# Optimization experiments

Hardware: AMD Instinct MI355X
Metric: run time of the kernel (lower is better)

## Reference

```python
import jax, jax.numpy as jnp
import numpy as np
from jax import lax

D_MODEL = 512
D_STATE = 16
D_CONV = 4
EXPAND = 2
D_INNER = EXPAND * D_MODEL          # 1024
DT_RANK = (D_MODEL + 15) // 16      # 32 (ceil(d_model/16))
BATCH = 8
SEQLEN = 2048


def _mamba_params(key):
    ks = jax.random.split(key, 6)
    s = 0.02
    return {
        'in_w':   jax.random.normal(ks[0], (2 * D_INNER, D_MODEL)) * s,
        'conv_w': jax.random.normal(ks[1], (D_INNER, D_CONV)) * s,
        'conv_b': jnp.zeros((D_INNER,)),
        'xp_w':   jax.random.normal(ks[2], (DT_RANK + 2 * D_STATE, D_INNER)) * s,
        'dt_w':   jax.random.normal(ks[3], (D_INNER, DT_RANK)) * s,
        'dt_b':   jax.random.uniform(ks[4], (D_INNER,), minval=-4.0, maxval=-2.0),
        'A_log':  jnp.log(jnp.tile(jnp.arange(1, D_STATE + 1, dtype=jnp.float32), (D_INNER, 1))),
        'Dp':     jnp.ones((D_INNER,)),
        'out_w':  jax.random.normal(ks[5], (D_MODEL, D_INNER)) * s,
    }


def setup_inputs() -> dict:
    key = jax.random.key(0)
    kx, kf, kb, kl1, kl2 = jax.random.split(key, 5)
    pf = _mamba_params(kf)
    pb = _mamba_params(kb)
    inp = {'x': jax.random.normal(kx, (BATCH, SEQLEN, D_MODEL), dtype=jnp.float32)}
    for name, v in pf.items():
        inp['f_' + name] = v
    for name, v in pb.items():
        inp['b_' + name] = v
    inp['lin_w'] = jax.random.normal(kl1, (D_MODEL, 2 * D_MODEL)) * 0.02
    inp['lin_b'] = jnp.zeros((D_MODEL,))
    return inp


def _mamba(x, in_w, conv_w, conv_b, xp_w, dt_w, dt_b, A_log, Dp, out_w):
    # x: (B, L, D_MODEL)
    Bsz = x.shape[0]
    xz = x @ in_w.T                                  # (B, L, 2*D_INNER)
    xi, z = jnp.split(xz, 2, axis=-1)
    # causal depthwise conv over time
    xc = jnp.transpose(xi, (0, 2, 1))                # (B, D_INNER, L)
    xc = lax.conv_general_dilated(
        xc, conv_w[:, None, :], (1,), [(D_CONV - 1, 0)],
        feature_group_count=D_INNER)
    xi = jax.nn.silu(jnp.transpose(xc + conv_b[None, :, None], (0, 2, 1)))
    # input-dependent SSM params
    dbl = xi @ xp_w.T                                # (B, L, DT_RANK + 2*N)
    dt = jax.nn.softplus(dbl[..., :DT_RANK] @ dt_w.T + dt_b)    # (B, L, D_INNER)
    Bm = dbl[..., DT_RANK:DT_RANK + D_STATE]                    # (B, L, N)
    Cm = dbl[..., DT_RANK + D_STATE:]                           # (B, L, N)
    A = -jnp.exp(A_log)                                         # (D_INNER, N)

    def step(h, inp):
        dt_t, B_t, C_t, x_t = inp                    # (B,Di), (B,N), (B,N), (B,Di)
        h = jnp.exp(dt_t[..., None] * A) * h + (dt_t * x_t)[..., None] * B_t[:, None, :]
        y = jnp.einsum('bdn,bn->bd', h, C_t)
        return h, y

    xs = (jnp.swapaxes(dt, 0, 1), jnp.swapaxes(Bm, 0, 1),
          jnp.swapaxes(Cm, 0, 1), jnp.swapaxes(xi, 0, 1))
    h0 = jnp.zeros((Bsz, D_INNER, D_STATE), dtype=x.dtype)
    _, ys = lax.scan(step, h0, xs)                   # ys: (L, B, D_INNER)
    y = jnp.swapaxes(ys, 0, 1) + xi * Dp
    y = y * jax.nn.silu(z)
    return y @ out_w.T                               # (B, L, D_MODEL)


def reference(x,
              f_in_w, f_conv_w, f_conv_b, f_xp_w, f_dt_w, f_dt_b, f_A_log, f_Dp, f_out_w,
              b_in_w, b_conv_w, b_conv_b, b_xp_w, b_dt_w, b_dt_b, b_A_log, b_Dp, b_out_w,
              lin_w, lin_b):
    y_fwd = _mamba(x, f_in_w, f_conv_w, f_conv_b, f_xp_w, f_dt_w, f_dt_b, f_A_log, f_Dp, f_out_w)
    y_bwd = _mamba(x[:, ::-1, :], b_in_w, b_conv_w, b_conv_b, b_xp_w, b_dt_w, b_dt_b,
                   b_A_log, b_Dp, b_out_w)[:, ::-1, :]
    y = jnp.concatenate([y_fwd, y_bwd], axis=-1)     # (B, L, 2*D_MODEL)
    return y @ lin_w.T + lin_b
```

## Files before the change

### kernel.cpp

```cpp
#include <hip/hip_runtime.h>
#include <cmath>

#define LSEQ 2048
#define NBATCH 8

typedef __attribute__((ext_vector_type(8))) short short8;
typedef __attribute__((ext_vector_type(4))) float f32x4;
typedef __attribute__((ext_vector_type(2))) float f32x2;

__device__ __forceinline__ float silu_f(float x) {
    return x * __builtin_amdgcn_rcpf(1.0f + __expf(-x));
}
__device__ __forceinline__ float softplus_f(float x) {
    return fmaxf(x, 0.0f) + __logf(1.0f + __expf(-fabsf(x)));
}
__device__ __forceinline__ unsigned short f2bf(float f) {
    unsigned int u = __float_as_uint(f);
    u += 0x7FFFu + ((u >> 16) & 1u);
    return (unsigned short)(u >> 16);
}
__device__ __forceinline__ float bf2f(unsigned short h) {
    return __uint_as_float(((unsigned int)h) << 16);
}
__device__ __forceinline__ void gload_lds16(const void* g, void* l) {
    __builtin_amdgcn_global_load_lds((const __attribute__((address_space(1))) void*)g,
                                     (__attribute__((address_space(3))) void*)l, 16, 0, 0);
}

#if defined(__has_builtin)
#if __has_builtin(__builtin_amdgcn_exp2f)
#define EXP2F(x) __builtin_amdgcn_exp2f(x)
#endif
#endif
#ifndef EXP2F
#define EXP2F(x) __expf((x) * 0.69314718055994531f)
#endif

struct GemmPair {
    const unsigned short* A[2];
    const unsigned short* A2[2];
    const unsigned short* W[2];
    const float* bias[2];
    void* C[2];
    void* Cz[2];
    unsigned short* aux[2];
};

template<int WGM, int WGN, int OMODE, int DK, int XTRA, int SPLIT = 0>
__global__ __launch_bounds__(WGM* WGN * 64) void gemm_mfma(GemmPair gp, int lda, int ldw,
                                                           int ldc, int K)
{
    constexpr int NW = WGM * WGN;
    constexpr int TM = WGM * 64, TN = WGN * 64;
    __shared__ unsigned short As[TM * 32];
    __shared__ unsigned short Bs[TN * 32];
    const int dir = blockIdx.z;
    const unsigned short* A  = gp.A[dir];
    const unsigned short* A2 = gp.A2[dir];
    const unsigned short* W  = gp.W[dir];
    const float* bias        = gp.bias[dir];
    void* Cout               = gp.C[dir];
    void* Czout              = gp.Cz[dir];
    unsigned short* aux      = gp.aux[dir];

    const int tid = threadIdx.x;
    const int wave = tid >> 6, lane = tid & 63;
    const int wm = wave / WGN, wn = wave % WGN;
    const int m0 = blockIdx.x * TM, n0 = blockIdx.y * TN;
    const int l15 = lane & 15, l4 = lane >> 4;
    const int srow = lane >> 2, schunk = (lane & 3) * 8;

    f32x4 acc[4][4] = {};

    for (int k0 = 0; k0 < K; k0 += 32) {
        __syncthreads();
        for (int s = wave; s < TM / 16; s += NW) {
            const int gr = m0 + s * 16 + srow;
            const unsigned short* g;
            if (DK != 0 && k0 >= DK)
                g = A2 + (size_t)(gr ^ (LSEQ - 1)) * lda + (k0 - DK) + schunk;
            else
                g = A + (size_t)gr * lda + k0 + schunk;
            gload_lds16(g, (char*)As + (size_t)s * 1024);
        }
        for (int s = wave; s < TN / 16; s += NW) {
            const int gr = n0 + s * 16 + srow;
            const unsigned short* g = W + (size_t)gr * ldw + k0 + schunk;
            gload_lds16(g, (char*)Bs + (size_t)s * 1024);
        }
        __syncthreads();
        short8 af[4], bfr[4];
#pragma unroll
        for (int mi = 0; mi < 4; ++mi)
            af[mi] = *(const short8*)&As[(wm * 64 + mi * 16 + l15) * 32 + l4 * 8];
#pragma unroll
        for (int ni = 0; ni < 4; ++ni)
            bfr[ni] = *(const short8*)&Bs[(wn * 64 + ni * 16 + l15) * 32 + l4 * 8];
#pragma unroll
        for (int mi = 0; mi < 4; ++mi)
#pragma unroll
            for (int ni = 0; ni < 4; ++ni)
                acc[mi][ni] = __builtin_amdgcn_mfma_f32_16x16x32_bf16(af[mi], bfr[ni], acc[mi][ni], 0, 0, 0);
    }

    void* Cb = (SPLIT && blockIdx.y * TN >= 1024) ? Czout : Cout;
#pragma unroll
    for (int mi = 0; mi < 4; ++mi)
#pragma unroll
        for (int ni = 0; ni < 4; ++ni)
#pragma unroll
            for (int r = 0; r < 4; ++r) {
                const int row = m0 + wm * 64 + mi * 16 + l4 * 4 + r;
                const int col = n0 + wn * 64 + ni * 16 + l15;
                const int colL = SPLIT ? (col & 1023) : col;
                float v = acc[mi][ni][r];
                if (bias) v += bias[col];
                if (OMODE & 1) ((unsigned short*)Cb)[(size_t)row * ldc + colL] = f2bf(v);
                else           ((float*)Cb)[(size_t)row * ldc + colL] = v;
                if (XTRA) { if (col < 32) aux[(size_t)row * 32 + col] = f2bf(v); }
            }
}

__global__ __launch_bounds__(256) void combine_k(
    const float* __restrict__ lin_w, const float* __restrict__ owf,
    const float* __restrict__ owb, unsigned short* __restrict__ Wcomb)
{
    const int dir = blockIdx.z;
    const float* ow = dir ? owb : owf;
    const int lane = threadIdx.x & 63;
    const int wave = threadIdx.x >> 6;
    const int n = blockIdx.y * 4 + wave;
    const int d = blockIdx.x * 256 + lane * 4;
    float4 acc = {0.f, 0.f, 0.f, 0.f};
    const float* lrow = lin_w + (size_t)n * 1024 + dir * 512;
    for (int j = 0; j < 512; ++j) {
        const float s = lrow[j];
        const float4 v = *(const float4*)&ow[(size_t)j * 1024 + d];
        acc.x = fmaf(s, v.x, acc.x); acc.y = fmaf(s, v.y, acc.y);
        acc.z = fmaf(s, v.z, acc.z); acc.w = fmaf(s, v.w, acc.w);
    }
    ushort4 o;
    o.x = f2bf(acc.x); o.y = f2bf(acc.y); o.z = f2bf(acc.z); o.w = f2bf(acc.w);
    *(ushort4*)&Wcomb[(size_t)n * 2048 + dir * 1024 + d] = o;
}

struct CvtArgs { const float* s[6]; unsigned short* d[6]; int n[6]; };
__global__ __launch_bounds__(256) void cvt_k(CvtArgs a)
{
    const int sid = blockIdx.y;
    const float* s = a.s[sid];
    unsigned short* d = a.d[sid];
    const int n4 = a.n[sid] >> 2;
    for (int i = blockIdx.x * 256 + threadIdx.x; i < n4; i += gridDim.x * 256) {
        const float4 v = ((const float4*)s)[i];
        ushort4 o; o.x = f2bf(v.x); o.y = f2bf(v.y); o.z = f2bf(v.z); o.w = f2bf(v.w);
        ((ushort4*)d)[i] = o;
    }
}
__global__ __launch_bounds__(256) void cvtx_k(const float* __restrict__ s,
                                              unsigned short* __restrict__ d, int n4)
{
    for (int i = blockIdx.x * 256 + threadIdx.x; i < n4; i += gridDim.x * 256) {
        const float4 v = ((const float4*)s)[i];
        ushort4 o; o.x = f2bf(v.x); o.y = f2bf(v.y); o.z = f2bf(v.z); o.w = f2bf(v.w);
        ((ushort4*)d)[i] = o;
    }
}

__global__ __launch_bounds__(256) void alprep_k(const float* __restrict__ af,
                                                const float* __restrict__ ab,
                                                float* __restrict__ of,
                                                float* __restrict__ ob)
{
    const int i = blockIdx.x * 256 + threadIdx.x;
    if (i < 16384) {
        of[i] = -expf(af[i]) * 1.4426950408889634f;
        ob[i] = -expf(ab[i]) * 1.4426950408889634f;
    }
}

__global__ __launch_bounds__(256) void conv_silu_k(
    const unsigned short* __restrict__ xc_f, const float* __restrict__ cw_f,
    const float* __restrict__ cb_f, unsigned short* __restrict__ xi_f,
    const unsigned short* __restrict__ xc_b, const float* __restrict__ cw_b,
    const float* __restrict__ cb_b, unsigned short* __restrict__ xi_b)
{
    const int dir = blockIdx.y;
    const unsigned short* xc = dir ? xc_b : xc_f;
    const float* cw = dir ? cw_b : cw_f;
    const float* cb = dir ? cb_b : cb_f;
    unsigned short* xi = dir ? xi_b : xi_f;

    const int bt = blockIdx.x;
    const int b = bt >> 11;
    const int t = bt & (LSEQ - 1);
    const int d = threadIdx.x << 2;

    float w[4][4];
#pragma unroll
    for (int i = 0; i < 4; ++i) {
        const float4 wr = *(const float4*)&cw[(d + i) * 4];
        w[i][0] = wr.x; w[i][1] = wr.y; w[i][2] = wr.z; w[i][3] = wr.w;
    }
    float4 acc = *(const float4*)&cb[d];
#pragma unroll
    for (int k = 0; k < 4; ++k) {
        const int row = dir ? (LSEQ - 1 - t) + 3 - k : t - 3 + k;
        if ((unsigned)row < (unsigned)LSEQ) {
            const ushort4 v = *(const ushort4*)&xc[(size_t)(b * LSEQ + row) * 1024 + d];
            acc.x += w[0][k] * bf2f(v.x); acc.y += w[1][k] * bf2f(v.y);
            acc.z += w[2][k] * bf2f(v.z); acc.w += w[3][k] * bf2f(v.w);
        }
    }
    ushort4 st;
    st.x = f2bf(silu_f(acc.x)); st.y = f2bf(silu_f(acc.y));
    st.z = f2bf(silu_f(acc.z)); st.w = f2bf(silu_f(acc.w));
    *(ushort4*)&xi[(size_t)(b * LSEQ + t) * 1024 + d] = st;
}

__device__ __forceinline__ float row_sum8(float x) {
    x += __int_as_float(__builtin_amdgcn_update_dpp(0, __float_as_int(x), 0xB1, 0xF, 0xF, true));
    x += __int_as_float(__builtin_amdgcn_update_dpp(0, __float_as_int(x), 0x4E, 0xF, 0xF, true));
    x += __int_as_float(__builtin_amdgcn_update_dpp(0, __float_as_int(x), 0x141, 0xF, 0xF, true));
    return x;
}

struct ScanPair {
    const unsigned short* dblh[2];
    const unsigned short* dtw[2];
    const float* dtb[2];
    unsigned short* xiy[2];
    const float* dbl[2];
    const unsigned short* zb[2];
    const float* Al[2];
    const float* Dp[2];
    float* cumg[2];
    float* he[2];
};

__global__ __launch_bounds__(256, 3) void scan_k(ScanPair sp)
{
    __shared__ unsigned short sxi[64][40];
    __shared__ float sdt[32][68], sdtx[32][68];
    __shared__ float sB2[8][140], sC2[8][140];
    __shared__ float sy[32][68];
    __shared__ float scum[32][68];

    const int dir = blockIdx.z;
    const unsigned short* dblh = sp.dblh[dir];
    const unsigned short* dtw  = sp.dtw[dir];
    const float* dtb           = sp.dtb[dir];
    unsigned short* xiy        = sp.xiy[dir];
    const float* dbl           = sp.dbl[dir];
    const unsigned short* zz   = sp.zb[dir];
    const float* Al            = sp.Al[dir];
    const float* Dpp           = sp.Dp[dir];
    float* cumg                = sp.cumg[dir];
    float* hep                 = sp.he[dir];

    const int by = blockIdx.y;
    const int b = by >> 1, part = by & 1;
    const int rbase = b * LSEQ + part * (LSEQ / 2);
    const int d0 = blockIdx.x << 5;
    const int tid = threadIdx.x;
    const int wave = tid >> 6, lane = tid & 63;
    const int l15 = lane & 15, l4 = lane >> 4;
    const int di = tid >> 3, np = tid & 7;
    const int lr = tid >> 2, lc = tid & 3;
    const bool lead = (np == 0);

    const f32x2 ALv = {-expf(Al[(d0 + di) * 16 + np]) * 1.4426950408889634f,
                       -expf(Al[(d0 + di) * 16 + np + 8]) * 1.4426950408889634f};

    const short8 dtwf0 = *(const short8*)&dtw[(size_t)(d0 + l15) * 32 + l4 * 8];
    const short8 dtwf1 = *(const short8*)&dtw[(size_t)(d0 + 16 + l15) * 32 + l4 * 8];
    const float dtb0 = dtb[d0 + l15], dtb1 = dtb[d0 + 16 + l15];

    float dpv[8];
#pragma unroll
    for (int i = 0; i < 8; ++i) dpv[i] = Dpp[d0 + lc * 8 + i];

    ushort4 pxi0, pxi1;
    float4 pB, pC;
    short8 pA;
    auto issue_loads = [&](int c) {
        const size_t r = (size_t)rbase + c * 64 + lr;
        pxi0 = *(const ushort4*)&xiy[r * 1024 + d0 + lc * 8];
        pxi1 = *(const ushort4*)&xiy[r * 1024 + d0 + lc * 8 + 4];
        pB   = *(const float4*)&dbl[r * 64 + 32 + lc * 4];
        pC   = *(const float4*)&dbl[r * 64 + 48 + lc * 4];
        pA   = *(const short8*)&dblh[(size_t)(rbase + c * 64 + wave * 16 + l15) * 32 + l4 * 8];
    };
    issue_loads(0);

    constexpr int NT = (LSEQ / 2) / 64;
    f32x2 h = {0.f, 0.f};
    float cum = 0.0f;
    for (int c = 0; c < NT; ++c) {
        const int t0 = c * 64;
        *(ushort4*)&sxi[lr][lc * 8]     = pxi0;
        *(ushort4*)&sxi[lr][lc * 8 + 4] = pxi1;
        {
            const float bv[4] = {pB.x, pB.y, pB.z, pB.w};
            const float cv[4] = {pC.x, pC.y, pC.z, pC.w};
#pragma unroll
            for (int i = 0; i < 4; ++i) {
                const int n = lc * 4 + i;
                sB2[n & 7][lr * 2 + (n >> 3)] = bv[i];
                sC2[n & 7][lr * 2 + (n >> 3)] = cv[i];
            }
        }
        __syncthreads();
        {
            f32x4 z4 = {0.f, 0.f, 0.f, 0.f};
            f32x4 dacc0 = __builtin_amdgcn_mfma_f32_16x16x32_bf16(pA, dtwf0, z4, 0, 0, 0);
            f32x4 dacc1 = __builtin_amdgcn_mfma_f32_16x16x32_bf16(pA, dtwf1, z4, 0, 0, 0);
            const int tq = wave * 16 + l4 * 4;
            float4 xi0, xi1;
            xi0.x = bf2f(sxi[tq + 0][l15]);      xi0.y = bf2f(sxi[tq + 1][l15]);
            xi0.z = bf2f(sxi[tq + 2][l15]);      xi0.w = bf2f(sxi[tq + 3][l15]);
            xi1.x = bf2f(sxi[tq + 0][16 + l15]); xi1.y = bf2f(sxi[tq + 1][16 + l15]);
            xi1.z = bf2f(sxi[tq + 2][16 + l15]); xi1.w = bf2f(sxi[tq + 3][16 + l15]);
            float4 dv0, dv1, dx0, dx1;
            dv0.x = softplus_f(dacc0[0] + dtb0); dv0.y = softplus_f(dacc0[1] + dtb0);
            dv0.z = softplus_f(dacc0[2] + dtb0); dv0.w = softplus_f(dacc0[3] + dtb0);
            dv1.x = softplus_f(dacc1[0] + dtb1); dv1.y = softplus_f(dacc1[1] + dtb1);
            dv1.z = softplus_f(dacc1[2] + dtb1); dv1.w = softplus_f(dacc1[3] + dtb1);
            dx0.x = dv0.x * xi0.x; dx0.y = dv0.y * xi0.y;
            dx0.z = dv0.z * xi0.z; dx0.w = dv0.w * xi0.w;
            dx1.x = dv1.x * xi1.x; dx1.y = dv1.y * xi1.y;
            dx1.z = dv1.z * xi1.z; dx1.w = dv1.w * xi1.w;
            *(float4*)&sdt[l15][tq]       = dv0;
            *(float4*)&sdt[16 + l15][tq]  = dv1;
            *(float4*)&sdtx[l15][tq]      = dx0;
            *(float4*)&sdtx[16 + l15][tq] = dx1;
        }
        const ushort4 oxi0 = pxi0, oxi1 = pxi1;
        ushort4 pz0 = {}, pz1 = {};
        if (part == 0) {
            const int tg = t0 + lr;
            const int tz = dir ? (LSEQ - 1 - tg) : tg;
            pz0 = *(const ushort4*)&zz[((size_t)b * LSEQ + tz) * 1024 + d0 + lc * 8];
            pz1 = *(const ushort4*)&zz[((size_t)b * LSEQ + tz) * 1024 + d0 + lc * 8 + 4];
        }
        if (c + 1 < NT) issue_loads(c + 1);
        __syncthreads();
#pragma unroll 4
        for (int tt = 0; tt < 64; tt += 4) {
            const float4 d4 = *(const float4*)&sdt[di][tt];
            const float4 u4 = *(const float4*)&sdtx[di][tt];
            const float4 bA = *(const float4*)&sB2[np][tt * 2];
            const float4 bB = *(const float4*)&sB2[np][tt * 2 + 4];
            const float4 cA = *(const float4*)&sC2[np][tt * 2];
            const float4 cB = *(const float4*)&sC2[np][tt * 2 + 4];
            float4 ppv;
            {
                f32x2 e = ALv * d4.x;
                e.x = EXP2F(e.x); e.y = EXP2F(e.y);
                const f32x2 b2 = {bA.x, bA.y};
                const f32x2 c2 = {cA.x, cA.y};
                h = e * h + b2 * u4.x;
                const f32x2 pc = h * c2;
                ppv.x = row_sum8(pc.x + pc.y);
            }
            {
                f32x2 e = ALv * d4.y;
                e.x = EXP2F(e.x); e.y = EXP2F(e.y);
                const f32x2 b2 = {bA.z, bA.w};
                const f32x2 c2 = {cA.z, cA.w};
                h = e * h + b2 * u4.y;
                const f32x2 pc = h * c2;
                ppv.y = row_sum8(pc.x + pc.y);
            }
            {
                f32x2 e = ALv * d4.z;
                e.x = EXP2F(e.x); e.y = EXP2F(e.y);
                const f32x2 b2 = {bB.x, bB.y};
                const f32x2 c2 = {cB.x, cB.y};
                h = e * h + b2 * u4.z;
                const f32x2 pc = h * c2;
                ppv.z = row_sum8(pc.x + pc.y);
            }
            {
                f32x2 e = ALv * d4.w;
                e.x = EXP2F(e.x); e.y = EXP2F(e.y);
                const f32x2 b2 = {bB.z, bB.w};
                const f32x2 c2 = {cB.z, cB.w};
                h = e * h + b2 * u4.w;
                const f32x2 pc = h * c2;
                ppv.w = row_sum8(pc.x + pc.y);
            }
            if (part) {
                const float c0 = cum + d4.x, c1 = c0 + d4.y;
                const float c2s = c1 + d4.z, c3 = c2s + d4.w;
                cum = c3;
                if (lead) {
                    float4 cc; cc.x = c0; cc.y = c1; cc.z = c2s; cc.w = c3;
                    *(float4*)&scum[di][tt] = cc;
                }
            }
            if (lead) *(float4*)&sy[di][tt] = ppv;
        }
        __syncthreads();
        if (part == 0) {
            const size_t r = (size_t)rbase + t0 + lr;
            ushort4 s0, s1;
            s0.x = f2bf(fmaf(bf2f(oxi0.x), dpv[0], sy[lc * 8 + 0][lr]) * silu_f(bf2f(pz0.x)));
            s0.y = f2bf(fmaf(bf2f(oxi0.y), dpv[1], sy[lc * 8 + 1][lr]) * silu_f(bf2f(pz0.y)));
            s0.z = f2bf(fmaf(bf2f(oxi0.z), dpv[2], sy[lc * 8 + 2][lr]) * silu_f(bf2f(pz0.z)));
            s0.w = f2bf(fmaf(bf2f(oxi0.w), dpv[3], sy[lc * 8 + 3][lr]) * silu_f(bf2f(pz0.w)));
            s1.x = f2bf(fmaf(bf2f(oxi1.x), dpv[4], sy[lc * 8 + 4][lr]) * silu_f(bf2f(pz1.x)));
            s1.y = f2bf(fmaf(bf2f(oxi1.y), dpv[5], sy[lc * 8 + 5][lr]) * silu_f(bf2f(pz1.y)));
            s1.z = f2bf(fmaf(bf2f(oxi1.z), dpv[6], sy[lc * 8 + 6][lr]) * silu_f(bf2f(pz1.z)));
            s1.w = f2bf(fmaf(bf2f(oxi1.w), dpv[7], sy[lc * 8 + 7][lr]) * silu_f(bf2f(pz1.w)));
            *(ushort4*)&xiy[r * 1024 + d0 + lc * 8] = s0;
            *(ushort4*)&xiy[r * 1024 + d0 + lc * 8 + 4] = s1;
        } else {
            const size_t r = (size_t)rbase + t0 + lr;
            ushort4 s0, s1;
            s0.x = f2bf(fmaf(bf2f(oxi0.x), dpv[0], sy[lc * 8 + 0][lr]));
            s0.y = f2bf(fmaf(bf2f(oxi0.y), dpv[1], sy[lc * 8 + 1][lr]));
            s0.z = f2bf(fmaf(bf2f(oxi0.z), dpv[2], sy[lc * 8 + 2][lr]));
            s0.w = f2bf(fmaf(bf2f(oxi0.w), dpv[3], sy[lc * 8 + 3][lr]));
            s1.x = f2bf(fmaf(bf2f(oxi1.x), dpv[4], sy[lc * 8 + 4][lr]));
            s1.y = f2bf(fmaf(bf2f(oxi1.y), dpv[5], sy[lc * 8 + 5][lr]));
            s1.z = f2bf(fmaf(bf2f(oxi1.z), dpv[6], sy[lc * 8 + 6][lr]));
            s1.w = f2bf(fmaf(bf2f(oxi1.w), dpv[7], sy[lc * 8 + 7][lr]));
            *(ushort4*)&xiy[r * 1024 + d0 + lc * 8] = s0;
            *(ushort4*)&xiy[r * 1024 + d0 + lc * 8 + 4] = s1;
            float4 c0v, c1v;
            c0v.x = scum[lc * 8 + 0][lr]; c0v.y = scum[lc * 8 + 1][lr];
            c0v.z = scum[lc * 8 + 2][lr]; c0v.w = scum[lc * 8 + 3][lr];
            c1v.x = scum[lc * 8 + 4][lr]; c1v.y = scum[lc * 8 + 5][lr];
            c1v.z = scum[lc * 8 + 6][lr]; c1v.w = scum[lc * 8 + 7][lr];
            const size_t pr = (size_t)(b * (LSEQ / 2) + t0 + lr) * 1024 + d0 + lc * 8;
            *(float4*)&cumg[pr]     = c0v;
            *(float4*)&cumg[pr + 4] = c1v;
        }
    }
    if (part == 0) {
        float* hh = &hep[((size_t)b * 1024 + d0 + di) * 16 + np];
        hh[0] = h.x; hh[8] = h.y;
    }
}

struct FixArgs {
    const float* cumg[2]; const float* he[2]; const float* al2[2];
    const float* dbl[2];  const unsigned short* zb[2]; unsigned short* xiy[2];
};
__global__ __launch_bounds__(256) void fix_k(FixArgs a)
{
    const int dir = blockIdx.z;
    const float* cumg          = a.cumg[dir];
    const float* he            = a.he[dir];
    const float* al2           = a.al2[dir];
    const float* dbl           = a.dbl[dir];
    const unsigned short* zz   = a.zb[dir];
    unsigned short* xiy        = a.xiy[dir];

    __shared__ float sAL[32][17], sHE[32][17];
    __shared__ float sCt[256][16];

    const int tid = threadIdx.x;
    const int d0 = blockIdx.x << 5;
    const int by = blockIdx.y;
    const int b = by >> 2, q = by & 3;
    const int tq0 = q << 8;

    for (int i = tid; i < 512; i += 256) {
        const int dd = i >> 4, nn = i & 15;
        sAL[dd][nn] = al2[(size_t)(d0 + dd) * 16 + nn];
        sHE[dd][nn] = he[((size_t)b * 1024 + d0 + dd) * 16 + nn];
    }
    for (int i = tid; i < 4096; i += 256) {
        const int tt = i >> 4, nn = i & 15;
        sCt[tt][nn] = dbl[((size_t)b * LSEQ + (LSEQ / 2) + tq0 + tt) * 64 + 48 + nn];
    }
    __syncthreads();

    const int ts = tid >> 5, dd = tid & 31;
    for (int it = 0; it < 32; ++it) {
        const int tl = tq0 + it * 8 + ts;
        const int tglob = (LSEQ / 2) + tl;
        const size_t grow = (size_t)b * LSEQ + tglob;
        const float cv = cumg[((size_t)b * (LSEQ / 2) + tl) * 1024 + d0 + dd];
        const float yv0 = bf2f(xiy[grow * 1024 + d0 + dd]);
        const int tz = dir ? (LSEQ - 1 - tglob) : tglob;
        const float z = bf2f(zz[((size_t)b * LSEQ + tz) * 1024 + d0 + dd]);
        float corr = 0.f;
#pragma unroll
        for (int n = 0; n < 16; ++n)
            corr = fmaf(sCt[it * 8 + ts][n] * sHE[dd][n], EXP2F(sAL[dd][n] * cv), corr);
        xiy[grow * 1024 + d0 + dd] = f2bf((yv0 + corr) * silu_f(z));
    }
}

extern "C" void kernel_launch(void* const* d_in, const int* in_sizes, int n_in,
                              void* d_out, int out_size, void* d_ws, size_t ws_size,
                              hipStream_t stream)
{
    const float* x      = (const float*)d_in[0];
    const float* f_in_w = (const float*)d_in[1];
    const float* f_cw   = (const float*)d_in[2];
    const float* f_cb   = (const float*)d_in[3];
    const float* f_xp   = (const float*)d_in[4];
    const float* f_dtw  = (const float*)d_in[5];
    const float* f_dtb  = (const float*)d_in[6];
    const float* f_Al   = (const float*)d_in[7];
    const float* f_Dp   = (const float*)d_in[8];
    const float* f_ow   = (const float*)d_in[9];
    const float* b_in_w = (const float*)d_in[10];
    const float* b_cw   = (const float*)d_in[11];
    const float* b_cb   = (const float*)d_in[12];
    const float* b_xp   = (const float*)d_in[13];
    const float* b_dtw  = (const float*)d_in[14];
    const float* b_dtb  = (const float*)d_in[15];
    const float* b_Al   = (const float*)d_in[16];
    const float* b_Dp   = (const float*)d_in[17];
    const float* b_ow   = (const float*)d_in[18];
    const float* lin_w  = (const float*)d_in[19];
    const float* lin_b  = (const float*)d_in[20];
    float* out = (float*)d_out;

    char* p = (char*)d_ws;
    auto take = [&](size_t bytes) -> char* {
        char* r = p; p += (bytes + 255) & ~(size_t)255; return r;
    };

    unsigned short* wif  = (unsigned short*)take((size_t)2048 * 512 * 2);
    unsigned short* wib  = (unsigned short*)take((size_t)2048 * 512 * 2);
    unsigned short* wxf  = (unsigned short*)take((size_t)64 * 1024 * 2);
    unsigned short* wxb  = (unsigned short*)take((size_t)64 * 1024 * 2);
    unsigned short* wdtf = (unsigned short*)take((size_t)1024 * 32 * 2);
    unsigned short* wdtb = (unsigned short*)take((size_t)1024 * 32 * 2);
    unsigned short* wcmb = (unsigned short*)take((size_t)512 * 2048 * 2);
    float* al2f = (float*)take((size_t)1024 * 16 * 4);
    float* al2b = (float*)take((size_t)1024 * 16 * 4);

    const size_t used = (size_t)(p - (char*)d_ws);
    const size_t perRow = 1024 + 2 * (2048 + 2048 + 2048 + 256 + 64);
    int G = 1;
    for (int g = 8; g >= 1; g >>= 1) {
        const size_t need = used + (size_t)g * LSEQ * perRow + (size_t)g * 2 * 1024 * 16 * 4 + 16384;
        if (need <= ws_size || g == 1) { G = g; break; }
    }

    CvtArgs ca;
    ca.s[0] = f_in_w; ca.d[0] = wif;  ca.n[0] = 2048 * 512;
    ca.s[1] = b_in_w; ca.d[1] = wib;  ca.n[1] = 2048 * 512;
    ca.s[2] = f_xp;   ca.d[2] = wxf;  ca.n[2] = 64 * 1024;
    ca.s[3] = b_xp;   ca.d[3] = wxb;  ca.n[3] = 64 * 1024;
    ca.s[4] = f_dtw;  ca.d[4] = wdtf; ca.n[4] = 1024 * 32;
    ca.s[5] = b_dtw;  ca.d[5] = wdtb; ca.n[5] = 1024 * 32;
    cvt_k<<<dim3(128, 6), 256, 0, stream>>>(ca);

    alprep_k<<<dim3(64), 256, 0, stream>>>(f_Al, b_Al, al2f, al2b);

    combine_k<<<dim3(4, 128, 2), 256, 0, stream>>>(lin_w, f_ow, b_ow, wcmb);

    char* pg0 = p;
    for (int g0 = 0; g0 < NBATCH; g0 += G) {
        const int Mg = G * LSEQ;
        p = pg0;
        unsigned short* xbf   = (unsigned short*)take((size_t)Mg * 512 * 2);
        unsigned short* xc_f  = (unsigned short*)take((size_t)Mg * 1024 * 2);
        unsigned short* zb_f  = (unsigned short*)take((size_t)Mg * 1024 * 2);
        unsigned short* xc_b  = (unsigned short*)take((size_t)Mg * 1024 * 2);
        unsigned short* zb_b  = (unsigned short*)take((size_t)Mg * 1024 * 2);
        unsigned short* xiy_f = (unsigned short*)take((size_t)Mg * 1024 * 2);
        unsigned short* xiy_b = (unsigned short*)take((size_t)Mg * 1024 * 2);
        float* dbl_f          = (float*)take((size_t)Mg * 64 * 4);
        float* dbl_b          = (float*)take((size_t)Mg * 64 * 4);
        unsigned short* dblh_f= (unsigned short*)take((size_t)Mg * 32 * 2);
        unsigned short* dblh_b= (unsigned short*)take((size_t)Mg * 32 * 2);
        float* he_f           = (float*)take((size_t)G * 1024 * 16 * 4);
        float* he_b           = (float*)take((size_t)G * 1024 * 16 * 4);
        float* cum_f = (float*)xc_f;
        float* cum_b = (float*)xc_b;

        const float* xg = x + (size_t)g0 * LSEQ * 512;
        float* outg = out + (size_t)g0 * LSEQ * 512;

        cvtx_k<<<dim3(512), 256, 0, stream>>>(xg, xbf, Mg * 512 / 4);

        GemmPair g1 = {};
        g1.A[0] = xbf; g1.A[1] = xbf; g1.W[0] = wif; g1.W[1] = wib;
        g1.C[0] = xc_f; g1.C[1] = xc_b; g1.Cz[0] = zb_f; g1.Cz[1] = zb_b;
        gemm_mfma<2,2,1,0,0,1><<<dim3(Mg/128, 16, 2), 256, 0, stream>>>(g1, 512, 512, 1024, 512);

        conv_silu_k<<<dim3(Mg, 2), 256, 0, stream>>>(xc_f, f_cw, f_cb, xiy_f,
                                                     xc_b, b_cw, b_cb, xiy_b);

        GemmPair g2 = {};
        g2.A[0] = xiy_f; g2.A[1] = xiy_b; g2.W[0] = wxf; g2.W[1] = wxb;
        g2.C[0] = dbl_f; g2.C[1] = dbl_b; g2.aux[0] = dblh_f; g2.aux[1] = dblh_b;
        gemm_mfma<4,1,0,0,1><<<dim3(Mg/256, 1, 2), 256, 0, stream>>>(g2, 1024, 1024, 64, 1024);

        ScanPair spp = {};
        spp.dblh[0] = dblh_f; spp.dblh[1] = dblh_b;
        spp.dtw[0] = wdtf;    spp.dtw[1] = wdtb;
        spp.dtb[0] = f_dtb;   spp.dtb[1] = b_dtb;
        spp.xiy[0] = xiy_f;   spp.xiy[1] = xiy_b;
        spp.dbl[0] = dbl_f;   spp.dbl[1] = dbl_b;
        spp.zb[0] = zb_f;     spp.zb[1] = zb_b;
        spp.Al[0] = f_Al;     spp.Al[1] = b_Al;
        spp.Dp[0] = f_Dp;     spp.Dp[1] = b_Dp;
        spp.cumg[0] = cum_f;  spp.cumg[1] = cum_b;
        spp.he[0] = he_f;     spp.he[1] = he_b;
        scan_k<<<dim3(32, G * 2, 2), 256, 0, stream>>>(spp);

        FixArgs fa = {};
        fa.cumg[0] = cum_f; fa.cumg[1] = cum_b;
        fa.he[0] = he_f;    fa.he[1] = he_b;
        fa.al2[0] = al2f;   fa.al2[1] = al2b;
        fa.dbl[0] = dbl_f;  fa.dbl[1] = dbl_b;
        fa.zb[0] = zb_f;    fa.zb[1] = zb_b;
        fa.xiy[0] = xiy_f;  fa.xiy[1] = xiy_b;
        fix_k<<<dim3(32, G * 4, 2), 256, 0, stream>>>(fa);

        GemmPair g5 = {};
        g5.A[0] = xiy_f; g5.A2[0] = xiy_b; g5.W[0] = wcmb;
        g5.bias[0] = lin_b; g5.C[0] = outg;
        gemm_mfma<2,2,0,1024,0><<<dim3(Mg/128, 4, 1), 256, 0, stream>>>(g5, 1024, 2048, 512, 2048);
    }
}
```

Before: 761.0 us.

## Compute four timesteps per conv thread, reuse scan LDS, shrink x_proj GEMM tiles

The depthwise conv kernel now has each thread produce four consecutive timesteps from seven loaded rows, so each row is read once instead of up to four times, and grid launches shrink fourfold. The scan kernel reuses the sdt/sdtx shared buffers for the y and cumulative outputs, cutting LDS so occupancy can rise to four blocks per CU. The x_proj GEMM switches to a smaller 128-thread tile configuration with twice as many blocks for better parallelism. Reusing sdt and sdtx relies on the existing barrier ordering to avoid races, and more registers per conv thread may reduce occupancy.

New measurement: 682.3 us. -10.3%, faster.

```diff
diff --git a/kernel.cpp b/kernel.cpp
--- a/kernel.cpp
+++ b/kernel.cpp
@@ -192,8 +192,8 @@
     unsigned short* xi = dir ? xi_b : xi_f;
 
     const int bt = blockIdx.x;
-    const int b = bt >> 11;
-    const int t = bt & (LSEQ - 1);
+    const int b = bt >> 9;
+    const int t0 = (bt & 511) << 2;
     const int d = threadIdx.x << 2;
 
     float w[4][4];
@@ -202,20 +202,33 @@
         const float4 wr = *(const float4*)&cw[(d + i) * 4];
         w[i][0] = wr.x; w[i][1] = wr.y; w[i][2] = wr.z; w[i][3] = wr.w;
     }
-    float4 acc = *(const float4*)&cb[d];
-#pragma unroll
-    for (int k = 0; k < 4; ++k) {
-        const int row = dir ? (LSEQ - 1 - t) + 3 - k : t - 3 + k;
+    const float4 bias = *(const float4*)&cb[d];
+
+    float4 r[7];
+#pragma unroll
+    for (int j = 0; j < 7; ++j) {
+        const int row = dir ? (LSEQ + 2 - t0 - j) : (t0 - 3 + j);
         if ((unsigned)row < (unsigned)LSEQ) {
             const ushort4 v = *(const ushort4*)&xc[(size_t)(b * LSEQ + row) * 1024 + d];
-            acc.x += w[0][k] * bf2f(v.x); acc.y += w[1][k] * bf2f(v.y);
-            acc.z += w[2][k] * bf2f(v.z); acc.w += w[3][k] * bf2f(v.w);
-        }
-    }
-    ushort4 st;
-    st.x = f2bf(silu_f(acc.x)); st.y = f2bf(silu_f(acc.y));
-    st.z = f2bf(silu_f(acc.z)); st.w = f2bf(silu_f(acc.w));
-    *(ushort4*)&xi[(size_t)(b * LSEQ + t) * 1024 + d] = st;
+            r[j].x = bf2f(v.x); r[j].y = bf2f(v.y); r[j].z = bf2f(v.z); r[j].w = bf2f(v.w);
+        } else {
+            r[j].x = 0.f; r[j].y = 0.f; r[j].z = 0.f; r[j].w = 0.f;
+        }
+    }
+#pragma unroll
+    for (int tt = 0; tt < 4; ++tt) {
+        float4 acc = bias;
+#pragma unroll
+        for (int k = 0; k < 4; ++k) {
+            const float4 v = r[tt + k];
+            acc.x += w[0][k] * v.x; acc.y += w[1][k] * v.y;
+            acc.z += w[2][k] * v.z; acc.w += w[3][k] * v.w;
+        }
+        ushort4 st;
+        st.x = f2bf(silu_f(acc.x)); st.y = f2bf(silu_f(acc.y));
+        st.z = f2bf(silu_f(acc.z)); st.w = f2bf(silu_f(acc.w));
+        *(ushort4*)&xi[(size_t)(b * LSEQ + t0 + tt) * 1024 + d] = st;
+    }
 }
 
 __device__ __forceinline__ float row_sum8(float x) {
@@ -238,13 +251,11 @@
     float* he[2];
 };
 
-__global__ __launch_bounds__(256, 3) void scan_k(ScanPair sp)
+__global__ __launch_bounds__(256, 4) void scan_k(ScanPair sp)
 {
     __shared__ unsigned short sxi[64][40];
     __shared__ float sdt[32][68], sdtx[32][68];
     __shared__ float sB2[8][140], sC2[8][140];
-    __shared__ float sy[32][68];
-    __shared__ float scum[32][68];
 
     const int dir = blockIdx.z;
     const unsigned short* dblh = sp.dblh[dir];
@@ -396,43 +407,43 @@
                 cum = c3;
                 if (lead) {
                     float4 cc; cc.x = c0; cc.y = c1; cc.z = c2s; cc.w = c3;
-                    *(float4*)&scum[di][tt] = cc;
+                    *(float4*)&sdt[di][tt] = cc;
                 }
             }
-            if (lead) *(float4*)&sy[di][tt] = ppv;
+            if (lead) *(float4*)&sdtx[di][tt] = ppv;
         }
         __syncthreads();
         if (part == 0) {
             const size_t r = (size_t)rbase + t0 + lr;
             ushort4 s0, s1;
-            s0.x = f2bf(fmaf(bf2f(oxi0.x), dpv[0], sy[lc * 8 + 0][lr]) * silu_f(bf2f(pz0.x)));
-            s0.y = f2bf(fmaf(bf2f(oxi0.y), dpv[1], sy[lc * 8 + 1][lr]) * silu_f(bf2f(pz0.y)));
-            s0.z = f2bf(fmaf(bf2f(oxi0.z), dpv[2], sy[lc * 8 + 2][lr]) * silu_f(bf2f(pz0.z)));
-            s0.w = f2bf(fmaf(bf2f(oxi0.w), dpv[3], sy[lc * 8 + 3][lr]) * silu_f(bf2f(pz0.w)));
-            s1.x = f2bf(fmaf(bf2f(oxi1.x), dpv[4], sy[lc * 8 + 4][lr]) * silu_f(bf2f(pz1.x)));
-            s1.y = f2bf(fmaf(bf2f(oxi1.y), dpv[5], sy[lc * 8 + 5][lr]) * silu_f(bf2f(pz1.y)));
-            s1.z = f2bf(fmaf(bf2f(oxi1.z), dpv[6], sy[lc * 8 + 6][lr]) * silu_f(bf2f(pz1.z)));
-            s1.w = f2bf(fmaf(bf2f(oxi1.w), dpv[7], sy[lc * 8 + 7][lr]) * silu_f(bf2f(pz1.w)));
+            s0.x = f2bf(fmaf(bf2f(oxi0.x), dpv[0], sdtx[lc * 8 + 0][lr]) * silu_f(bf2f(pz0.x)));
+            s0.y = f2bf(fmaf(bf2f(oxi0.y), dpv[1], sdtx[lc * 8 + 1][lr]) * silu_f(bf2f(pz0.y)));
+            s0.z = f2bf(fmaf(bf2f(oxi0.z), dpv[2], sdtx[lc * 8 + 2][lr]) * silu_f(bf2f(pz0.z)));
+            s0.w = f2bf(fmaf(bf2f(oxi0.w), dpv[3], sdtx[lc * 8 + 3][lr]) * silu_f(bf2f(pz0.w)));
+            s1.x = f2bf(fmaf(bf2f(oxi1.x), dpv[4], sdtx[lc * 8 + 4][lr]) * silu_f(bf2f(pz1.x)));
+            s1.y = f2bf(fmaf(bf2f(oxi1.y), dpv[5], sdtx[lc * 8 + 5][lr]) * silu_f(bf2f(pz1.y)));
+            s1.z = f2bf(fmaf(bf2f(oxi1.z), dpv[6], sdtx[lc * 8 + 6][lr]) * silu_f(bf2f(pz1.z)));
+            s1.w = f2bf(fmaf(bf2f(oxi1.w), dpv[7], sdtx[lc * 8 + 7][lr]) * silu_f(bf2f(pz1.w)));
             *(ushort4*)&xiy[r * 1024 + d0 + lc * 8] = s0;
             *(ushort4*)&xiy[r * 1024 + d0 + lc * 8 + 4] = s1;
         } else {
             const size_t r = (size_t)rbase + t0 + lr;
             ushort4 s0, s1;
-            s0.x = f2bf(fmaf(bf2f(oxi0.x), dpv[0], sy[lc * 8 + 0][lr]));
-            s0.y = f2bf(fmaf(bf2f(oxi0.y), dpv[1], sy[lc * 8 + 1][lr]));
-            s0.z = f2bf(fmaf(bf2f(oxi0.z), dpv[2], sy[lc * 8 + 2][lr]));
-            s0.w = f2bf(fmaf(bf2f(oxi0.w), dpv[3], sy[lc * 8 + 3][lr]));
-            s1.x = f2bf(fmaf(bf2f(oxi1.x), dpv[4], sy[lc * 8 + 4][lr]));
-            s1.y = f2bf(fmaf(bf2f(oxi1.y), dpv[5], sy[lc * 8 + 5][lr]));
-            s1.z = f2bf(fmaf(bf2f(oxi1.z), dpv[6], sy[lc * 8 + 6][lr]));
-            s1.w = f2bf(fmaf(bf2f(oxi1.w), dpv[7], sy[lc * 8 + 7][lr]));
+            s0.x = f2bf(fmaf(bf2f(oxi0.x), dpv[0], sdtx[lc * 8 + 0][lr]));
+            s0.y = f2bf(fmaf(bf2f(oxi0.y), dpv[1], sdtx[lc * 8 + 1][lr]));
+            s0.z = f2bf(fmaf(bf2f(oxi0.z), dpv[2], sdtx[lc * 8 + 2][lr]));
+            s0.w = f2bf(fmaf(bf2f(oxi0.w), dpv[3], sdtx[lc * 8 + 3][lr]));
+            s1.x = f2bf(fmaf(bf2f(oxi1.x), dpv[4], sdtx[lc * 8 + 4][lr]));
+            s1.y = f2bf(fmaf(bf2f(oxi1.y), dpv[5], sdtx[lc * 8 + 5][lr]));
+            s1.z = f2bf(fmaf(bf2f(oxi1.z), dpv[6], sdtx[lc * 8 + 6][lr]));
+            s1.w = f2bf(fmaf(bf2f(oxi1.w), dpv[7], sdtx[lc * 8 + 7][lr]));
             *(ushort4*)&xiy[r * 1024 + d0 + lc * 8] = s0;
             *(ushort4*)&xiy[r * 1024 + d0 + lc * 8 + 4] = s1;
             float4 c0v, c1v;
-            c0v.x = scum[lc * 8 + 0][lr]; c0v.y = scum[lc * 8 + 1][lr];
-            c0v.z = scum[lc * 8 + 2][lr]; c0v.w = scum[lc * 8 + 3][lr];
-            c1v.x = scum[lc * 8 + 4][lr]; c1v.y = scum[lc * 8 + 5][lr];
-            c1v.z = scum[lc * 8 + 6][lr]; c1v.w = scum[lc * 8 + 7][lr];
+            c0v.x = sdt[lc * 8 + 0][lr]; c0v.y = sdt[lc * 8 + 1][lr];
+            c0v.z = sdt[lc * 8 + 2][lr]; c0v.w = sdt[lc * 8 + 3][lr];
+            c1v.x = sdt[lc * 8 + 4][lr]; c1v.y = sdt[lc * 8 + 5][lr];
+            c1v.z = sdt[lc * 8 + 6][lr]; c1v.w = sdt[lc * 8 + 7][lr];
             const size_t pr = (size_t)(b * (LSEQ / 2) + t0 + lr) * 1024 + d0 + lc * 8;
             *(float4*)&cumg[pr]     = c0v;
             *(float4*)&cumg[pr + 4] = c1v;
@@ -588,13 +599,13 @@
         g1.C[0] = xc_f; g1.C[1] = xc_b; g1.Cz[0] = zb_f; g1.Cz[1] = zb_b;
         gemm_mfma<2,2,1,0,0,1><<<dim3(Mg/128, 16, 2), 256, 0, stream>>>(g1, 512, 512, 1024, 512);
 
-        conv_silu_k<<<dim3(Mg, 2), 256, 0, stream>>>(xc_f, f_cw, f_cb, xiy_f,
-                                                     xc_b, b_cw, b_cb, xiy_b);
+        conv_silu_k<<<dim3(Mg/4, 2), 256, 0, stream>>>(xc_f, f_cw, f_cb, xiy_f,
+                                                       xc_b, b_cw, b_cb, xiy_b);
 
         GemmPair g2 = {};
         g2.A[0] = xiy_f; g2.A[1] = xiy_b; g2.W[0] = wxf; g2.W[1] = wxb;
         g2.C[0] = dbl_f; g2.C[1] = dbl_b; g2.aux[0] = dblh_f; g2.aux[1] = dblh_b;
-        gemm_mfma<4,1,0,0,1><<<dim3(Mg/256, 1, 2), 256, 0, stream>>>(g2, 1024, 1024, 64, 1024);
+        gemm_mfma<2,1,0,0,1><<<dim3(Mg/128, 1, 2), 128, 0, stream>>>(g2, 1024, 1024, 64, 1024);
 
         ScanPair spp = {};
         spp.dblh[0] = dblh_f; spp.dblh[1] = dblh_b;
```

## Tile conv over 8 timesteps, raise scan occupancy, vectorize fixup, retile x_proj GEMM

Applied to the files above, without the earlier changes.

The depthwise conv kernel now has each thread produce 8 consecutive timesteps from 11 loaded rows, so overlapping inputs are reused instead of re-read per timestep, and it launches 8x fewer blocks. The scan kernel drops a shared buffer by reusing sdt for cumulative sums and raises its launch bound to 4 blocks per CU. It also skips one __syncthreads when part==0, which looks like it could open a race on the shared staging buffers. The fixup loop processes two channels per thread with vectorized loads and stores, and the x_proj GEMM moves to smaller 128-row tiles with 128 threads to get more blocks.

Result: faster. 661.7 us (-13.1%).

```diff
diff --git a/kernel.cpp b/kernel.cpp
--- a/kernel.cpp
+++ b/kernel.cpp
@@ -192,8 +192,8 @@
     unsigned short* xi = dir ? xi_b : xi_f;
 
     const int bt = blockIdx.x;
-    const int b = bt >> 11;
-    const int t = bt & (LSEQ - 1);
+    const int b = bt >> 8;
+    const int t0 = (bt & 255) << 3;
     const int d = threadIdx.x << 2;
 
     float w[4][4];
@@ -202,20 +202,33 @@
         const float4 wr = *(const float4*)&cw[(d + i) * 4];
         w[i][0] = wr.x; w[i][1] = wr.y; w[i][2] = wr.z; w[i][3] = wr.w;
     }
-    float4 acc = *(const float4*)&cb[d];
-#pragma unroll
-    for (int k = 0; k < 4; ++k) {
-        const int row = dir ? (LSEQ - 1 - t) + 3 - k : t - 3 + k;
+    const float4 bias = *(const float4*)&cb[d];
+
+    float4 r[11];
+#pragma unroll
+    for (int j = 0; j < 11; ++j) {
+        const int row = dir ? (LSEQ + 2 - t0 - j) : (t0 - 3 + j);
         if ((unsigned)row < (unsigned)LSEQ) {
             const ushort4 v = *(const ushort4*)&xc[(size_t)(b * LSEQ + row) * 1024 + d];
-            acc.x += w[0][k] * bf2f(v.x); acc.y += w[1][k] * bf2f(v.y);
-            acc.z += w[2][k] * bf2f(v.z); acc.w += w[3][k] * bf2f(v.w);
-        }
-    }
-    ushort4 st;
-    st.x = f2bf(silu_f(acc.x)); st.y = f2bf(silu_f(acc.y));
-    st.z = f2bf(silu_f(acc.z)); st.w = f2bf(silu_f(acc.w));
-    *(ushort4*)&xi[(size_t)(b * LSEQ + t) * 1024 + d] = st;
+            r[j].x = bf2f(v.x); r[j].y = bf2f(v.y); r[j].z = bf2f(v.z); r[j].w = bf2f(v.w);
+        } else {
+            r[j].x = 0.f; r[j].y = 0.f; r[j].z = 0.f; r[j].w = 0.f;
+        }
+    }
+#pragma unroll
+    for (int tt = 0; tt < 8; ++tt) {
+        float4 acc = bias;
+#pragma unroll
+        for (int k = 0; k < 4; ++k) {
+            const float4 v = r[tt + k];
+            acc.x += w[0][k] * v.x; acc.y += w[1][k] * v.y;
+            acc.z += w[2][k] * v.z; acc.w += w[3][k] * v.w;
+        }
+        ushort4 st;
+        st.x = f2bf(silu_f(acc.x)); st.y = f2bf(silu_f(acc.y));
+        st.z = f2bf(silu_f(acc.z)); st.w = f2bf(silu_f(acc.w));
+        *(ushort4*)&xi[(size_t)(b * LSEQ + t0 + tt) * 1024 + d] = st;
+    }
 }
 
 __device__ __forceinline__ float row_sum8(float x) {
@@ -238,13 +251,12 @@
     float* he[2];
 };
 
-__global__ __launch_bounds__(256, 3) void scan_k(ScanPair sp)
+__global__ __launch_bounds__(256, 4) void scan_k(ScanPair sp)
 {
     __shared__ unsigned short sxi[64][40];
     __shared__ float sdt[32][68], sdtx[32][68];
     __shared__ float sB2[8][140], sC2[8][140];
-    __shared__ float sy[32][68];
-    __shared__ float scum[32][68];
+    __shared__ float sy[32][66];
 
     const int dir = blockIdx.z;
     const unsigned short* dblh = sp.dblh[dir];
@@ -310,7 +322,7 @@
                 sC2[n & 7][lr * 2 + (n >> 3)] = cv[i];
             }
         }
-        __syncthreads();
+        if (part) __syncthreads();
         {
             f32x4 z4 = {0.f, 0.f, 0.f, 0.f};
             f32x4 dacc0 = __builtin_amdgcn_mfma_f32_16x16x32_bf16(pA, dtwf0, z4, 0, 0, 0);
@@ -396,7 +408,7 @@
                 cum = c3;
                 if (lead) {
                     float4 cc; cc.x = c0; cc.y = c1; cc.z = c2s; cc.w = c3;
-                    *(float4*)&scum[di][tt] = cc;
+                    *(float4*)&sdt[di][tt] = cc;
                 }
             }
             if (lead) *(float4*)&sy[di][tt] = ppv;
@@ -429,10 +441,10 @@
             *(ushort4*)&xiy[r * 1024 + d0 + lc * 8] = s0;
             *(ushort4*)&xiy[r * 1024 + d0 + lc * 8 + 4] = s1;
             float4 c0v, c1v;
-            c0v.x = scum[lc * 8 + 0][lr]; c0v.y = scum[lc * 8 + 1][lr];
-            c0v.z = scum[lc * 8 + 2][lr]; c0v.w = scum[lc * 8 + 3][lr];
-            c1v.x = scum[lc * 8 + 4][lr]; c1v.y = scum[lc * 8 + 5][lr];
-            c1v.z = scum[lc * 8 + 6][lr]; c1v.w = scum[lc * 8 + 7][lr];
+            c0v.x = sdt[lc * 8 + 0][lr]; c0v.y = sdt[lc * 8 + 1][lr];
+            c0v.z = sdt[lc * 8 + 2][lr]; c0v.w = sdt[lc * 8 + 3][lr];
+            c1v.x = sdt[lc * 8 + 4][lr]; c1v.y = sdt[lc * 8 + 5][lr];
+            c1v.z = sdt[lc * 8 + 6][lr]; c1v.w = sdt[lc * 8 + 7][lr];
             const size_t pr = (size_t)(b * (LSEQ / 2) + t0 + lr) * 1024 + d0 + lc * 8;
             *(float4*)&cumg[pr]     = c0v;
             *(float4*)&cumg[pr + 4] = c1v;
@@ -478,20 +490,27 @@
     }
     __syncthreads();
 
-    const int ts = tid >> 5, dd = tid & 31;
-    for (int it = 0; it < 32; ++it) {
-        const int tl = tq0 + it * 8 + ts;
+    const int ts = tid >> 4, dd = (tid & 15) * 2;
+    for (int it = 0; it < 16; ++it) {
+        const int tloc = it * 16 + ts;
+        const int tl = tq0 + tloc;
         const int tglob = (LSEQ / 2) + tl;
         const size_t grow = (size_t)b * LSEQ + tglob;
-        const float cv = cumg[((size_t)b * (LSEQ / 2) + tl) * 1024 + d0 + dd];
-        const float yv0 = bf2f(xiy[grow * 1024 + d0 + dd]);
+        const float2 cv = *(const float2*)&cumg[((size_t)b * (LSEQ / 2) + tl) * 1024 + d0 + dd];
+        const ushort2 yv = *(const ushort2*)&xiy[grow * 1024 + d0 + dd];
         const int tz = dir ? (LSEQ - 1 - tglob) : tglob;
-        const float z = bf2f(zz[((size_t)b * LSEQ + tz) * 1024 + d0 + dd]);
-        float corr = 0.f;
-#pragma unroll
-        for (int n = 0; n < 16; ++n)
-            corr = fmaf(sCt[it * 8 + ts][n] * sHE[dd][n], EXP2F(sAL[dd][n] * cv), corr);
-        xiy[grow * 1024 + d0 + dd] = f2bf((yv0 + corr) * silu_f(z));
+        const ushort2 zv = *(const ushort2*)&zz[((size_t)b * LSEQ + tz) * 1024 + d0 + dd];
+        float corr0 = 0.f, corr1 = 0.f;
+#pragma unroll
+        for (int n = 0; n < 16; ++n) {
+            const float ct = sCt[tloc][n];
+            corr0 = fmaf(ct * sHE[dd + 0][n], EXP2F(sAL[dd + 0][n] * cv.x), corr0);
+            corr1 = fmaf(ct * sHE[dd + 1][n], EXP2F(sAL[dd + 1][n] * cv.y), corr1);
+        }
+        ushort2 o;
+        o.x = f2bf((bf2f(yv.x) + corr0) * silu_f(bf2f(zv.x)));
+        o.y = f2bf((bf2f(yv.y) + corr1) * silu_f(bf2f(zv.y)));
+        *(ushort2*)&xiy[grow * 1024 + d0 + dd] = o;
     }
 }
 
@@ -588,13 +607,13 @@
         g1.C[0] = xc_f; g1.C[1] = xc_b; g1.Cz[0] = zb_f; g1.Cz[1] = zb_b;
         gemm_mfma<2,2,1,0,0,1><<<dim3(Mg/128, 16, 2), 256, 0, stream>>>(g1, 512, 512, 1024, 512);
 
-        conv_silu_k<<<dim3(Mg, 2), 256, 0, stream>>>(xc_f, f_cw, f_cb, xiy_f,
-                                                     xc_b, b_cw, b_cb, xiy_b);
+        conv_silu_k<<<dim3(Mg/8, 2), 256, 0, stream>>>(xc_f, f_cw, f_cb, xiy_f,
+                                                       xc_b, b_cw, b_cb, xiy_b);
 
         GemmPair g2 = {};
         g2.A[0] = xiy_f; g2.A[1] = xiy_b; g2.W[0] = wxf; g2.W[1] = wxb;
         g2.C[0] = dbl_f; g2.C[1] = dbl_b; g2.aux[0] = dblh_f; g2.aux[1] = dblh_b;
-        gemm_mfma<4,1,0,0,1><<<dim3(Mg/256, 1, 2), 256, 0, stream>>>(g2, 1024, 1024, 64, 1024);
+        gemm_mfma<2,1,0,0,1><<<dim3(Mg/128, 1, 2), 128, 0, stream>>>(g2, 1024, 1024, 64, 1024);
 
         ScanPair spp = {};
         spp.dblh[0] = dblh_f; spp.dblh[1] = dblh_b;
```
